# Performance work log

Hardware: AMD Instinct MI355X
Metric: run time of the kernel (lower is better)

The kernel has to match this reference:

```python
import jax, jax.numpy as jnp
import numpy as np

B, H, S, D = 2, 16, 2048, 64

def setup_inputs() -> dict:
    key = jax.random.key(0)
    k1, k2, k3 = jax.random.split(key, 3)
    Q = jax.random.normal(k1, (B, H, S, D), dtype=jnp.float32)
    K = jax.random.normal(k2, (B, H, S, D), dtype=jnp.float32)
    V = jax.random.normal(k3, (B, H, S, D), dtype=jnp.float32)
    mask = jnp.zeros((S, S), dtype=bool)  # original default: all-False mask
    return {"Q": Q, "K": K, "V": V, "mask": mask}

def reference(Q, K, V, mask) -> jnp.ndarray:
    # Faithful to the original: dk is the KEY SEQUENCE LENGTH (K.size(-2)),
    # and masked_fill(-1e10) happens BEFORE dividing by sqrt(dk).
    dk = K.shape[-2]
    scores = jnp.einsum('bhqd,bhkd->bhqk', Q, K)          # [B,H,S,S]
    scores = jnp.where(mask, -1e10, scores) / jnp.sqrt(jnp.float32(dk))
    attn = jax.nn.softmax(scores, axis=-1)
    return jnp.einsum('bhqk,bhkd->bhqd', attn, V)
```

## Files before the change

### kernel.cpp

```cpp
#include <hip/hip_runtime.h>

#define SQ   2048
#define DD   64
#define BK   64
#define BQ   128
#define LDW  72
#define NT   32

typedef _Float16 f16x8 __attribute__((ext_vector_type(8)));
typedef _Float16 f16x4 __attribute__((ext_vector_type(4)));
typedef float    f32x4 __attribute__((ext_vector_type(4)));

__global__ __launch_bounds__(256, 2)
void attn_fused3(const float* __restrict__ Qg,
                 const float* __restrict__ Kg,
                 const float* __restrict__ Vg,
                 const unsigned char* __restrict__ maskg,
                 float* __restrict__ Og)
{
    __shared__ _Float16 Kl[2][BK * LDW];
    __shared__ _Float16 Vt[2][DD * LDW];

    const int tid  = threadIdx.x;
    const int lane = tid & 63;
    const int w    = tid >> 6;
    const int quad = lane >> 4;
    const int l16  = lane & 15;

    const int n     = blockIdx.x;
    const int bh    = (n & 7) + 8 * ((n >> 3) & 3);
    const int qtile = n >> 5;
    const int qBase = qtile * BQ;

    const float scale  = 0.02209708691207961f;
    const float MASKED = -1e10f * 0.02209708691207961f;

    f16x8 qf[2][2];
#pragma unroll
    for (int qg = 0; qg < 2; ++qg) {
        const float* qrow = Qg + ((size_t)bh * SQ + qBase + w * 32 + qg * 16 + l16) * DD;
#pragma unroll
        for (int h = 0; h < 2; ++h) {
            float4 a = *(const float4*)(qrow + h * 32 + quad * 8);
            float4 b = *(const float4*)(qrow + h * 32 + quad * 8 + 4);
            qf[qg][h][0] = (_Float16)(a.x * scale); qf[qg][h][1] = (_Float16)(a.y * scale);
            qf[qg][h][2] = (_Float16)(a.z * scale); qf[qg][h][3] = (_Float16)(a.w * scale);
            qf[qg][h][4] = (_Float16)(b.x * scale); qf[qg][h][5] = (_Float16)(b.y * scale);
            qf[qg][h][6] = (_Float16)(b.z * scale); qf[qg][h][7] = (_Float16)(b.w * scale);
        }
    }

    f32x4 acc[2][4];
#pragma unroll
    for (int qg = 0; qg < 2; ++qg)
#pragma unroll
        for (int d = 0; d < 4; ++d) acc[qg][d] = (f32x4){0.f, 0.f, 0.f, 0.f};
    float lsum[2] = {0.f, 0.f};

    const int sr  = tid >> 2;
    const int sc4 = (tid & 3) * 16;
    const int vq  = tid & 15;
    const int vdb = (tid >> 4) * 4;
    const int ctw  = vq >> 2, qdw = vq & 3;
    const int keyp = (ctw >> 1) * 32 + qdw * 8 + (ctw & 1) * 4;

    const float* Kbase = Kg + (size_t)bh * SQ * DD;
    const float* Vbase = Vg + (size_t)bh * SQ * DD;
    const unsigned char* mbase = maskg + (size_t)(qBase + (tid >> 1)) * SQ + (tid & 1) * 32;

    {
        const float* ks = Kbase + (size_t)sr * DD + sc4;
        float4 k0v = *(const float4*)(ks + 0), k1v = *(const float4*)(ks + 4);
        float4 k2v = *(const float4*)(ks + 8), k3v = *(const float4*)(ks + 12);
        float4 v0, v1, v2, v3;
        v0 = *(const float4*)(Vbase + (size_t)(vq * 4 + 0) * DD + vdb);
        v1 = *(const float4*)(Vbase + (size_t)(vq * 4 + 1) * DD + vdb);
        v2 = *(const float4*)(Vbase + (size_t)(vq * 4 + 2) * DD + vdb);
        v3 = *(const float4*)(Vbase + (size_t)(vq * 4 + 3) * DD + vdb);
        f16x8 y0, y1;
        y0[0]=(_Float16)k0v.x; y0[1]=(_Float16)k0v.y; y0[2]=(_Float16)k0v.z; y0[3]=(_Float16)k0v.w;
        y0[4]=(_Float16)k1v.x; y0[5]=(_Float16)k1v.y; y0[6]=(_Float16)k1v.z; y0[7]=(_Float16)k1v.w;
        y1[0]=(_Float16)k2v.x; y1[1]=(_Float16)k2v.y; y1[2]=(_Float16)k2v.z; y1[3]=(_Float16)k2v.w;
        y1[4]=(_Float16)k3v.x; y1[5]=(_Float16)k3v.y; y1[6]=(_Float16)k3v.z; y1[7]=(_Float16)k3v.w;
        *(f16x8*)&Kl[0][sr * LDW + sc4]     = y0;
        *(f16x8*)&Kl[0][sr * LDW + sc4 + 8] = y1;
        f16x4 t0 = {(_Float16)v0.x,(_Float16)v1.x,(_Float16)v2.x,(_Float16)v3.x};
        f16x4 t1 = {(_Float16)v0.y,(_Float16)v1.y,(_Float16)v2.y,(_Float16)v3.y};
        f16x4 t2 = {(_Float16)v0.z,(_Float16)v1.z,(_Float16)v2.z,(_Float16)v3.z};
        f16x4 t3 = {(_Float16)v0.w,(_Float16)v1.w,(_Float16)v2.w,(_Float16)v3.w};
        *(f16x4*)&Vt[0][(vdb + 0) * LDW + keyp] = t0;
        *(f16x4*)&Vt[0][(vdb + 1) * LDW + keyp] = t1;
        *(f16x4*)&Vt[0][(vdb + 2) * LDW + keyp] = t2;
        *(f16x4*)&Vt[0][(vdb + 3) * LDW + keyp] = t3;
    }
    uint4 ma = *(const uint4*)(mbase), mb = *(const uint4*)(mbase + 16);
    int tm = __syncthreads_or((int)(ma.x | ma.y | ma.z | ma.w | mb.x | mb.y | mb.z | mb.w));

#pragma unroll 2
    for (int kt = 0; kt < NT; ++kt) {
        const int cur = kt & 1;
        const bool more = (kt + 1 < NT);

        float4 kx[4], vx[4]; uint4 ma2 = {0,0,0,0}, mb2 = {0,0,0,0};
        if (more) {
            const int k0n = (kt + 1) * BK;
            const float* ks = Kbase + (size_t)(k0n + sr) * DD + sc4;
            kx[0] = *(const float4*)(ks + 0);  kx[1] = *(const float4*)(ks + 4);
            kx[2] = *(const float4*)(ks + 8);  kx[3] = *(const float4*)(ks + 12);
            const float* vb = Vbase + (size_t)(k0n + vq * 4) * DD + vdb;
            vx[0] = *(const float4*)(vb);           vx[1] = *(const float4*)(vb + DD);
            vx[2] = *(const float4*)(vb + 2 * DD);  vx[3] = *(const float4*)(vb + 3 * DD);
            ma2 = *(const uint4*)(mbase + k0n);
            mb2 = *(const uint4*)(mbase + k0n + 16);
        }

        f32x4 sA[4], sB[4];
#pragma unroll
        for (int ct = 0; ct < 4; ++ct) {
            f16x8 kf0 = *(const f16x8*)&Kl[cur][(ct * 16 + l16) * LDW + quad * 8];
            f16x8 kf1 = *(const f16x8*)&Kl[cur][(ct * 16 + l16) * LDW + 32 + quad * 8];
            f32x4 c0 = (f32x4){0.f, 0.f, 0.f, 0.f};
            c0 = __builtin_amdgcn_mfma_f32_16x16x32_f16(kf0, qf[0][0], c0, 0, 0, 0);
            c0 = __builtin_amdgcn_mfma_f32_16x16x32_f16(kf1, qf[0][1], c0, 0, 0, 0);
            sA[ct] = c0;
            f32x4 c1 = (f32x4){0.f, 0.f, 0.f, 0.f};
            c1 = __builtin_amdgcn_mfma_f32_16x16x32_f16(kf0, qf[1][0], c1, 0, 0, 0);
            c1 = __builtin_amdgcn_mfma_f32_16x16x32_f16(kf1, qf[1][1], c1, 0, 0, 0);
            sB[ct] = c1;
        }

        if (tm) {
#pragma unroll
            for (int qg = 0; qg < 2; ++qg) {
                const int qgq = qBase + w * 32 + qg * 16 + l16;
#pragma unroll
                for (int ct = 0; ct < 4; ++ct)
#pragma unroll
                    for (int r = 0; r < 4; ++r) {
                        const int kg = kt * BK + ct * 16 + quad * 4 + r;
                        if (maskg[(size_t)qgq * SQ + kg]) {
                            if (qg == 0) sA[ct][r] = MASKED; else sB[ct][r] = MASKED;
                        }
                    }
            }
        }

        f16x4 pA[4], pB[4];
        float ls0 = 0.f, ls1 = 0.f;
#pragma unroll
        for (int ct = 0; ct < 4; ++ct) {
#pragma unroll
            for (int r = 0; r < 4; ++r) {
                const float ea = __expf(sA[ct][r]);
                const float eb = __expf(sB[ct][r]);
                ls0 += ea; ls1 += eb;
                pA[ct][r] = (_Float16)ea;
                pB[ct][r] = (_Float16)eb;
            }
        }
        lsum[0] += ls0; lsum[1] += ls1;

#pragma unroll
        for (int dt = 0; dt < 4; ++dt) {
#pragma unroll
            for (int cp = 0; cp < 2; ++cp) {
                f16x8 vv = *(const f16x8*)&Vt[cur][(dt * 16 + l16) * LDW + cp * 32 + quad * 8];
                f16x4 vlo = {vv[0], vv[1], vv[2], vv[3]};
                f16x4 vhi = {vv[4], vv[5], vv[6], vv[7]};
                acc[0][dt] = __builtin_amdgcn_mfma_f32_16x16x16f16(pA[cp*2+0], vlo, acc[0][dt], 0, 0, 0);
                acc[0][dt] = __builtin_amdgcn_mfma_f32_16x16x16f16(pA[cp*2+1], vhi, acc[0][dt], 0, 0, 0);
                acc[1][dt] = __builtin_amdgcn_mfma_f32_16x16x16f16(pB[cp*2+0], vlo, acc[1][dt], 0, 0, 0);
                acc[1][dt] = __builtin_amdgcn_mfma_f32_16x16x16f16(pB[cp*2+1], vhi, acc[1][dt], 0, 0, 0);
            }
        }

        if (more) {
            f16x8 y0, y1;
            y0[0]=(_Float16)kx[0].x; y0[1]=(_Float16)kx[0].y; y0[2]=(_Float16)kx[0].z; y0[3]=(_Float16)kx[0].w;
            y0[4]=(_Float16)kx[1].x; y0[5]=(_Float16)kx[1].y; y0[6]=(_Float16)kx[1].z; y0[7]=(_Float16)kx[1].w;
            y1[0]=(_Float16)kx[2].x; y1[1]=(_Float16)kx[2].y; y1[2]=(_Float16)kx[2].z; y1[3]=(_Float16)kx[2].w;
            y1[4]=(_Float16)kx[3].x; y1[5]=(_Float16)kx[3].y; y1[6]=(_Float16)kx[3].z; y1[7]=(_Float16)kx[3].w;
            *(f16x8*)&Kl[cur ^ 1][sr * LDW + sc4]     = y0;
            *(f16x8*)&Kl[cur ^ 1][sr * LDW + sc4 + 8] = y1;
            f16x4 t0 = {(_Float16)vx[0].x,(_Float16)vx[1].x,(_Float16)vx[2].x,(_Float16)vx[3].x};
            f16x4 t1 = {(_Float16)vx[0].y,(_Float16)vx[1].y,(_Float16)vx[2].y,(_Float16)vx[3].y};
            f16x4 t2 = {(_Float16)vx[0].z,(_Float16)vx[1].z,(_Float16)vx[2].z,(_Float16)vx[3].z};
            f16x4 t3 = {(_Float16)vx[0].w,(_Float16)vx[1].w,(_Float16)vx[2].w,(_Float16)vx[3].w};
            *(f16x4*)&Vt[cur ^ 1][(vdb + 0) * LDW + keyp] = t0;
            *(f16x4*)&Vt[cur ^ 1][(vdb + 1) * LDW + keyp] = t1;
            *(f16x4*)&Vt[cur ^ 1][(vdb + 2) * LDW + keyp] = t2;
            *(f16x4*)&Vt[cur ^ 1][(vdb + 3) * LDW + keyp] = t3;
        }
        tm = __syncthreads_or((int)(ma2.x | ma2.y | ma2.z | ma2.w | mb2.x | mb2.y | mb2.z | mb2.w));
    }

#pragma unroll
    for (int qg = 0; qg < 2; ++qg) {
        float l = lsum[qg];
        l += __shfl_xor(l, 16);
        l += __shfl_xor(l, 32);
        float lrow[4];
#pragma unroll
        for (int r = 0; r < 4; ++r) lrow[r] = __shfl(l, quad * 4 + r);
        float* ob = Og + ((size_t)bh * SQ + qBase + w * 32 + qg * 16) * DD;
#pragma unroll
        for (int r = 0; r < 4; ++r) {
            const float inv = 1.0f / lrow[r];
            const int qr = quad * 4 + r;
#pragma unroll
            for (int dt = 0; dt < 4; ++dt)
                ob[qr * DD + dt * 16 + l16] = acc[qg][dt][r] * inv;
        }
    }
}

extern "C" void kernel_launch(void* const* d_in, const int* in_sizes, int n_in,
                              void* d_out, int out_size, void* d_ws, size_t ws_size,
                              hipStream_t stream) {
    const float* Q = (const float*)d_in[0];
    const float* K = (const float*)d_in[1];
    const float* V = (const float*)d_in[2];
    const unsigned char* mask = (const unsigned char*)d_in[3];
    float* Out = (float*)d_out;
    attn_fused3<<<dim3(32 * 16), dim3(256), 0, stream>>>(Q, K, V, mask, Out);
}
```

Baseline: 159.4 us.

## Split key range across two blocks with combine kernel, use exp2 and wider MFMA

```diff
diff --git a/kernel.cpp b/kernel.cpp
--- a/kernel.cpp
+++ b/kernel.cpp
@@ -5,18 +5,24 @@
 #define BK   64
 #define BQ   128
 #define LDW  72
-#define NT   32
+#define NBH  32
 
 typedef _Float16 f16x8 __attribute__((ext_vector_type(8)));
 typedef _Float16 f16x4 __attribute__((ext_vector_type(4)));
 typedef float    f32x4 __attribute__((ext_vector_type(4)));
 
-__global__ __launch_bounds__(256, 2)
-void attn_fused3(const float* __restrict__ Qg,
-                 const float* __restrict__ Kg,
-                 const float* __restrict__ Vg,
-                 const unsigned char* __restrict__ maskg,
-                 float* __restrict__ Og)
+#define SCALE_LOG2E ((float)(0.02209708691207961 * 1.4426950408889634))
+#define MASKED_VAL  (-1e10f * SCALE_LOG2E)
+
+template<bool SPLIT>
+__global__ __launch_bounds__(256, 4)
+void attn_fa(const float* __restrict__ Qg,
+             const float* __restrict__ Kg,
+             const float* __restrict__ Vg,
+             const unsigned char* __restrict__ maskg,
+             float* __restrict__ Og,
+             float* __restrict__ wsAcc,
+             float* __restrict__ wsL)
 {
     __shared__ _Float16 Kl[2][BK * LDW];
     __shared__ _Float16 Vt[2][DD * LDW];
@@ -27,13 +33,13 @@
     const int quad = lane >> 4;
     const int l16  = lane & 15;
 
-    const int n     = blockIdx.x;
-    const int bh    = (n & 7) + 8 * ((n >> 3) & 3);
-    const int qtile = n >> 5;
+    const int n    = blockIdx.x;
+    const int bh   = (n & 7) + 8 * ((n >> 3) & 3);
+    const int half = SPLIT ? ((n >> 5) & 1) : 0;
+    const int qtile = SPLIT ? (n >> 6) : (n >> 5);
     const int qBase = qtile * BQ;
-
-    const float scale  = 0.02209708691207961f;
-    const float MASKED = -1e10f * 0.02209708691207961f;
+    const int kt0  = SPLIT ? half * 16 : 0;
+    const int KTN  = SPLIT ? 16 : 32;
 
     f16x8 qf[2][2];
 #pragma unroll
@@ -43,10 +49,10 @@
         for (int h = 0; h < 2; ++h) {
             float4 a = *(const float4*)(qrow + h * 32 + quad * 8);
             float4 b = *(const float4*)(qrow + h * 32 + quad * 8 + 4);
-            qf[qg][h][0] = (_Float16)(a.x * scale); qf[qg][h][1] = (_Float16)(a.y * scale);
-            qf[qg][h][2] = (_Float16)(a.z * scale); qf[qg][h][3] = (_Float16)(a.w * scale);
-            qf[qg][h][4] = (_Float16)(b.x * scale); qf[qg][h][5] = (_Float16)(b.y * scale);
-            qf[qg][h][6] = (_Float16)(b.z * scale); qf[qg][h][7] = (_Float16)(b.w * scale);
+            qf[qg][h][0] = (_Float16)(a.x * SCALE_LOG2E); qf[qg][h][1] = (_Float16)(a.y * SCALE_LOG2E);
+            qf[qg][h][2] = (_Float16)(a.z * SCALE_LOG2E); qf[qg][h][3] = (_Float16)(a.w * SCALE_LOG2E);
+            qf[qg][h][4] = (_Float16)(b.x * SCALE_LOG2E); qf[qg][h][5] = (_Float16)(b.y * SCALE_LOG2E);
+            qf[qg][h][6] = (_Float16)(b.z * SCALE_LOG2E); qf[qg][h][7] = (_Float16)(b.w * SCALE_LOG2E);
         }
     }
 
@@ -61,7 +67,7 @@
     const int sc4 = (tid & 3) * 16;
     const int vq  = tid & 15;
     const int vdb = (tid >> 4) * 4;
-    const int ctw  = vq >> 2, qdw = vq & 3;
+    const int ctw = vq >> 2, qdw = vq & 3;
     const int keyp = (ctw >> 1) * 32 + qdw * 8 + (ctw & 1) * 4;
 
     const float* Kbase = Kg + (size_t)bh * SQ * DD;
@@ -69,14 +75,12 @@
     const unsigned char* mbase = maskg + (size_t)(qBase + (tid >> 1)) * SQ + (tid & 1) * 32;
 
     {
-        const float* ks = Kbase + (size_t)sr * DD + sc4;
+        const float* ks = Kbase + (size_t)(kt0 * BK + sr) * DD + sc4;
         float4 k0v = *(const float4*)(ks + 0), k1v = *(const float4*)(ks + 4);
         float4 k2v = *(const float4*)(ks + 8), k3v = *(const float4*)(ks + 12);
-        float4 v0, v1, v2, v3;
-        v0 = *(const float4*)(Vbase + (size_t)(vq * 4 + 0) * DD + vdb);
-        v1 = *(const float4*)(Vbase + (size_t)(vq * 4 + 1) * DD + vdb);
-        v2 = *(const float4*)(Vbase + (size_t)(vq * 4 + 2) * DD + vdb);
-        v3 = *(const float4*)(Vbase + (size_t)(vq * 4 + 3) * DD + vdb);
+        const float* vb = Vbase + (size_t)(kt0 * BK + vq * 4) * DD + vdb;
+        float4 v0 = *(const float4*)(vb);          float4 v1 = *(const float4*)(vb + DD);
+        float4 v2 = *(const float4*)(vb + 2 * DD); float4 v3 = *(const float4*)(vb + 3 * DD);
         f16x8 y0, y1;
         y0[0]=(_Float16)k0v.x; y0[1]=(_Float16)k0v.y; y0[2]=(_Float16)k0v.z; y0[3]=(_Float16)k0v.w;
         y0[4]=(_Float16)k1v.x; y0[5]=(_Float16)k1v.y; y0[6]=(_Float16)k1v.z; y0[7]=(_Float16)k1v.w;
@@ -93,13 +97,14 @@
         *(f16x4*)&Vt[0][(vdb + 2) * LDW + keyp] = t2;
         *(f16x4*)&Vt[0][(vdb + 3) * LDW + keyp] = t3;
     }
-    uint4 ma = *(const uint4*)(mbase), mb = *(const uint4*)(mbase + 16);
+    uint4 ma = *(const uint4*)(mbase + kt0 * BK), mb = *(const uint4*)(mbase + kt0 * BK + 16);
     int tm = __syncthreads_or((int)(ma.x | ma.y | ma.z | ma.w | mb.x | mb.y | mb.z | mb.w));
 
 #pragma unroll 2
-    for (int kt = 0; kt < NT; ++kt) {
-        const int cur = kt & 1;
-        const bool more = (kt + 1 < NT);
+    for (int idx = 0; idx < KTN; ++idx) {
+        const int kt  = kt0 + idx;
+        const int cur = idx & 1;
+        const bool more = (idx + 1 < KTN);
 
         float4 kx[4], vx[4]; uint4 ma2 = {0,0,0,0}, mb2 = {0,0,0,0};
         if (more) {
@@ -139,40 +144,35 @@
                     for (int r = 0; r < 4; ++r) {
                         const int kg = kt * BK + ct * 16 + quad * 4 + r;
                         if (maskg[(size_t)qgq * SQ + kg]) {
-                            if (qg == 0) sA[ct][r] = MASKED; else sB[ct][r] = MASKED;
+                            if (qg == 0) sA[ct][r] = MASKED_VAL; else sB[ct][r] = MASKED_VAL;
                         }
                     }
             }
         }
 
-        f16x4 pA[4], pB[4];
+        f16x8 pA[2], pB[2];
         float ls0 = 0.f, ls1 = 0.f;
 #pragma unroll
-        for (int ct = 0; ct < 4; ++ct) {
-#pragma unroll
-            for (int r = 0; r < 4; ++r) {
-                const float ea = __expf(sA[ct][r]);
-                const float eb = __expf(sB[ct][r]);
+        for (int kb = 0; kb < 2; ++kb)
+#pragma unroll
+            for (int j = 0; j < 8; ++j) {
+                const int ct = kb * 2 + (j >> 2), r = j & 3;
+                const float ea = __builtin_amdgcn_exp2f(sA[ct][r]);
+                const float eb = __builtin_amdgcn_exp2f(sB[ct][r]);
                 ls0 += ea; ls1 += eb;
-                pA[ct][r] = (_Float16)ea;
-                pB[ct][r] = (_Float16)eb;
-            }
-        }
+                pA[kb][j] = (_Float16)ea;
+                pB[kb][j] = (_Float16)eb;
+            }
         lsum[0] += ls0; lsum[1] += ls1;
 
 #pragma unroll
-        for (int dt = 0; dt < 4; ++dt) {
-#pragma unroll
-            for (int cp = 0; cp < 2; ++cp) {
-                f16x8 vv = *(const f16x8*)&Vt[cur][(dt * 16 + l16) * LDW + cp * 32 + quad * 8];
-                f16x4 vlo = {vv[0], vv[1], vv[2], vv[3]};
-                f16x4 vhi = {vv[4], vv[5], vv[6], vv[7]};
-                acc[0][dt] = __builtin_amdgcn_mfma_f32_16x16x16f16(pA[cp*2+0], vlo, acc[0][dt], 0, 0, 0);
-                acc[0][dt] = __builtin_amdgcn_mfma_f32_16x16x16f16(pA[cp*2+1], vhi, acc[0][dt], 0, 0, 0);
-                acc[1][dt] = __builtin_amdgcn_mfma_f32_16x16x16f16(pB[cp*2+0], vlo, acc[1][dt], 0, 0, 0);
-                acc[1][dt] = __builtin_amdgcn_mfma_f32_16x16x16f16(pB[cp*2+1], vhi, acc[1][dt], 0, 0, 0);
-            }
-        }
+        for (int dt = 0; dt < 4; ++dt)
+#pragma unroll
+            for (int kb = 0; kb < 2; ++kb) {
+                f16x8 vv = *(const f16x8*)&Vt[cur][(dt * 16 + l16) * LDW + kb * 32 + quad * 8];
+                acc[0][dt] = __builtin_amdgcn_mfma_f32_16x16x32_f16(pA[kb], vv, acc[0][dt], 0, 0, 0);
+                acc[1][dt] = __builtin_amdgcn_mfma_f32_16x16x32_f16(pB[kb], vv, acc[1][dt], 0, 0, 0);
+            }
 
         if (more) {
             f16x8 y0, y1;
@@ -199,19 +199,52 @@
         float l = lsum[qg];
         l += __shfl_xor(l, 16);
         l += __shfl_xor(l, 32);
-        float lrow[4];
-#pragma unroll
-        for (int r = 0; r < 4; ++r) lrow[r] = __shfl(l, quad * 4 + r);
-        float* ob = Og + ((size_t)bh * SQ + qBase + w * 32 + qg * 16) * DD;
-#pragma unroll
-        for (int r = 0; r < 4; ++r) {
-            const float inv = 1.0f / lrow[r];
-            const int qr = quad * 4 + r;
-#pragma unroll
-            for (int dt = 0; dt < 4; ++dt)
-                ob[qr * DD + dt * 16 + l16] = acc[qg][dt][r] * inv;
-        }
-    }
+        if (SPLIT) {
+            float* ob = wsAcc + (((size_t)half * NBH + bh) * SQ + qBase + w * 32 + qg * 16) * DD;
+#pragma unroll
+            for (int r = 0; r < 4; ++r) {
+                const int qr = quad * 4 + r;
+#pragma unroll
+                for (int dt = 0; dt < 4; ++dt)
+                    ob[qr * DD + dt * 16 + l16] = acc[qg][dt][r];
+            }
+            if (quad == 0)
+                wsL[((size_t)half * NBH + bh) * SQ + qBase + w * 32 + qg * 16 + l16] = l;
+        } else {
+            float lrow[4];
+#pragma unroll
+            for (int r = 0; r < 4; ++r) lrow[r] = __shfl(l, quad * 4 + r);
+            float* ob = Og + ((size_t)bh * SQ + qBase + w * 32 + qg * 16) * DD;
+#pragma unroll
+            for (int r = 0; r < 4; ++r) {
+                const float inv = 1.0f / lrow[r];
+                const int qr = quad * 4 + r;
+#pragma unroll
+                for (int dt = 0; dt < 4; ++dt)
+                    ob[qr * DD + dt * 16 + l16] = acc[qg][dt][r] * inv;
+            }
+        }
+    }
+}
+
+__global__ __launch_bounds__(256)
+void attn_combine(const float* __restrict__ wsAcc,
+                  const float* __restrict__ wsL,
+                  float* __restrict__ Og)
+{
+    const int G   = blockIdx.x * 256 + threadIdx.x;
+    const int row = G >> 4;
+    const int c   = G & 15;
+    const size_t HALF4 = (size_t)NBH * SQ * (DD / 4);
+    float4 a0 = ((const float4*)wsAcc)[(size_t)row * 16 + c];
+    float4 a1 = ((const float4*)wsAcc)[HALF4 + (size_t)row * 16 + c];
+    const float inv = 1.0f / (wsL[row] + wsL[(size_t)NBH * SQ + row]);
+    float4 o;
+    o.x = (a0.x + a1.x) * inv;
+    o.y = (a0.y + a1.y) * inv;
+    o.z = (a0.z + a1.z) * inv;
+    o.w = (a0.w + a1.w) * inv;
+    ((float4*)Og)[(size_t)row * 16 + c] = o;
 }
 
 extern "C" void kernel_launch(void* const* d_in, const int* in_sizes, int n_in,
@@ -222,5 +255,17 @@
     const float* V = (const float*)d_in[2];
     const unsigned char* mask = (const unsigned char*)d_in[3];
     float* Out = (float*)d_out;
-    attn_fused3<<<dim3(32 * 16), dim3(256), 0, stream>>>(Q, K, V, mask, Out);
+
+    const size_t accFloats = (size_t)2 * NBH * SQ * DD;
+    const size_t lFloats   = (size_t)2 * NBH * SQ;
+    const size_t needBytes = (accFloats + lFloats) * sizeof(float);
+
+    if (ws_size >= needBytes) {
+        float* wsAcc = (float*)d_ws;
+        float* wsL   = wsAcc + accFloats;
+        attn_fa<true><<<dim3(32 * 16 * 2), dim3(256), 0, stream>>>(Q, K, V, mask, Out, wsAcc, wsL);
+        attn_combine<<<dim3((NBH * SQ * (DD / 4)) / 256), dim3(256), 0, stream>>>(wsAcc, wsL, Out);
+    } else {
+        attn_fa<false><<<dim3(32 * 16), dim3(256), 0, stream>>>(Q, K, V, mask, Out, nullptr, nullptr);
+    }
 }
```

Result: slower. 420.0 us (+163.4%).
